# Kernel tuning notes

Measured on AMD Instinct MI355X. Metric: run time of the kernel, lower is better.

The kernel has to match this reference:

```python
import jax, jax.numpy as jnp
import numpy as np

B, S, D, H, FF = 2, 2048, 512, 8, 2048
DK = D // H
EPS = 1e-5


def layer_norm(x, g, b):
    mu = jnp.mean(x, axis=-1, keepdims=True)
    var = jnp.mean((x - mu) ** 2, axis=-1, keepdims=True)
    return (x - mu) / jnp.sqrt(var + EPS) * g + b


def split_heads(x):  # [B,S,D] -> [B,H,S,DK]
    b, s, _ = x.shape
    return x.reshape(b, s, H, DK).transpose(0, 2, 1, 3)


def merge_heads(x):  # [B,H,S,DK] -> [B,S,D]
    b, h, s, dk = x.shape
    return x.transpose(0, 2, 1, 3).reshape(b, s, h * dk)


def mha(q_in, kv, in_w, in_b, out_w, out_b):
    # torch nn.MultiheadAttention, batch_first, eval mode (no dropout)
    Wq, Wk, Wv = in_w[:D], in_w[D:2 * D], in_w[2 * D:]
    bq, bk, bv = in_b[:D], in_b[D:2 * D], in_b[2 * D:]
    q = split_heads(q_in @ Wq.T + bq)
    k = split_heads(kv @ Wk.T + bk)
    v = split_heads(kv @ Wv.T + bv)
    scores = jnp.einsum('bhqd,bhkd->bhqk', q, k) / jnp.sqrt(jnp.float32(DK))
    attn = jax.nn.softmax(scores, axis=-1)
    out = merge_heads(jnp.einsum('bhqk,bhkd->bhqd', attn, v))
    return out @ out_w.T + out_b


def setup_inputs() -> dict:
    key = jax.random.key(0)
    ks = jax.random.split(key, 32)
    p = lambda k, shape: (jax.random.normal(k, shape, jnp.float32) * 0.02)
    inp = {
        'x_q': jax.random.normal(ks[0], (B, S, D), jnp.float32),
        'x1': jax.random.normal(ks[1], (B, S, D), jnp.float32),
        'x2': jax.random.normal(ks[2], (B, S, D), jnp.float32),
        # causal self-attention projections (no output proj in original)
        'sa_wq': p(ks[3], (D, D)), 'sa_bq': jnp.zeros((D,), jnp.float32),
        'sa_wk': p(ks[4], (D, D)), 'sa_bk': jnp.zeros((D,), jnp.float32),
        'sa_wv': p(ks[5], (D, D)), 'sa_bv': jnp.zeros((D,), jnp.float32),
        'ln1_g': jnp.ones((D,), jnp.float32), 'ln1_b': jnp.zeros((D,), jnp.float32),
        # shared cross-attention (cross_attn used twice in forward)
        'mha_in_w': p(ks[6], (3 * D, D)), 'mha_in_b': jnp.zeros((3 * D,), jnp.float32),
        'mha_out_w': p(ks[7], (D, D)), 'mha_out_b': jnp.zeros((D,), jnp.float32),
        # shared add_norm2 (used twice)
        'ln2_g': jnp.ones((D,), jnp.float32), 'ln2_b': jnp.zeros((D,), jnp.float32),
        # FFN
        'ffn_w1': p(ks[8], (FF, D)), 'ffn_b1': jnp.zeros((FF,), jnp.float32),
        'ffn_w2': p(ks[9], (D, FF)), 'ffn_b2': jnp.zeros((D,), jnp.float32),
        # add_norm3 (final)
        'ln3_g': jnp.ones((D,), jnp.float32), 'ln3_b': jnp.zeros((D,), jnp.float32),
    }
    return inp


def reference(x_q, x1, x2, sa_wq, sa_bq, sa_wk, sa_bk, sa_wv, sa_bv,
              ln1_g, ln1_b, mha_in_w, mha_in_b, mha_out_w, mha_out_b,
              ln2_g, ln2_b, ffn_w1, ffn_b1, ffn_w2, ffn_b2, ln3_g, ln3_b):
    # --- causal self-attention (hand-rolled, masked_fill with -1e9) ---
    q = split_heads(x_q @ sa_wq.T + sa_bq)
    k = split_heads(x_q @ sa_wk.T + sa_bk)
    v = split_heads(x_q @ sa_wv.T + sa_bv)
    scores = jnp.einsum('bhqd,bhkd->bhqk', q, k) / jnp.sqrt(jnp.float32(DK))
    causal = jnp.tril(jnp.ones((S, S), dtype=bool))
    scores = jnp.where(causal[None, None], scores, jnp.float32(-1e9))
    attn = jax.nn.softmax(scores, axis=-1)
    y_sa = merge_heads(jnp.einsum('bhqk,bhkd->bhqd', attn, v))
    y = layer_norm(x_q + y_sa, ln1_g, ln1_b)
    # --- cross-attention 1 (shared weights) + shared add_norm2 ---
    yattn = mha(y, x1, mha_in_w, mha_in_b, mha_out_w, mha_out_b)
    yattn = layer_norm(y + yattn, ln2_g, ln2_b)
    # --- cross-attention 2 (SAME module/weights as cross-attn 1) ---
    yattn2 = mha(yattn, x2, mha_in_w, mha_in_b, mha_out_w, mha_out_b)
    yattn2 = layer_norm(yattn + yattn2, ln2_g, ln2_b)
    # --- FFN + add_norm3 ---
    h = jax.nn.relu(yattn2 @ ffn_w1.T + ffn_b1)
    ff = h @ ffn_w2.T + ffn_b2
    return layer_norm(yattn2 + ff, ln3_g, ln3_b)
```

## Files before the change

kernel.cpp:

```cpp
#include <hip/hip_runtime.h>
#include <hip/hip_bf16.h>

#define S_LEN 2048
#define DMODEL 512
#define NHEAD 8
#define DKH 64
#define FFDIM 2048
#define BATCH 2
#define NROWS (BATCH * S_LEN)

using bf16 = __hip_bfloat16;
typedef __bf16 bf16x8 __attribute__((ext_vector_type(8)));
typedef float floatx4 __attribute__((ext_vector_type(4)));
typedef float floatx16 __attribute__((ext_vector_type(16)));

__device__ inline unsigned short f2bf_bits(float f) {
    union { float f; unsigned u; } c; c.f = f;
    return (unsigned short)((c.u + 0x7FFFu + ((c.u >> 16) & 1u)) >> 16);
}
__device__ inline unsigned pack2bf(float a, float b) {
    return (unsigned)f2bf_bits(a) | ((unsigned)f2bf_bits(b) << 16);
}
__device__ inline unsigned pk2(float a, float b) {
    float2 f; f.x = a; f.y = b;
    __hip_bfloat162 h = __float22bfloat162_rn(f);
    return *(unsigned*)&h;
}

__device__ __forceinline__ void gload_lds16(const bf16* g, bf16* l) {
    __builtin_amdgcn_global_load_lds(
        (const __attribute__((address_space(1))) void*)(const void*)g,
        (__attribute__((address_space(3))) void*)(void*)l, 16, 0, 0);
}

struct CvtSeg { const float* s; bf16* d; int n4; };
struct CvtDesc { CvtSeg seg[12]; };

__launch_bounds__(256)
__global__ void cvt_f32_bf16(CvtDesc desc) {
    const CvtSeg sg = desc.seg[blockIdx.y];
    const int stride = gridDim.x * 256;
    for (int i = blockIdx.x * 256 + threadIdx.x; i < sg.n4; i += stride) {
        const float4 v = ((const float4*)sg.s)[i];
        uint2 o;
        o.x = pack2bf(v.x, v.y);
        o.y = pack2bf(v.z, v.w);
        ((uint2*)sg.d)[i] = o;
    }
}

struct Epi {
    bf16*  outB[3];
    float* outF[3];
    const float* bias[3];
    float scale[3];
    const bf16* A2;
    int a2slab;
    int shift;
    int relu;
};

template <int BM, int BN>
__launch_bounds__(256)
__global__ void gemm2(const bf16* __restrict__ A, const bf16* __restrict__ W,
                      Epi epi, int K)
{
    constexpr int WR = BM / 32;
    constexpr int WC = BN / 32;
    constexpr int SA = BM / 16;
    constexpr int SB = BN / 16;
    constexpr int NG = 2 * (SA + SB);

    __shared__ alignas(16) bf16 As[2][BM][32];
    __shared__ alignas(16) bf16 Bs[2][BN][32];

    const int t = threadIdx.x;
    const int w = t >> 6;
    const int lane = t & 63;
    const int r16 = lane & 15;
    const int quad = lane >> 4;
    const int wm = w >> 1, wn = w & 1;
    const int m0 = blockIdx.x * BM;
    const int n0 = blockIdx.y * BN;

    const bf16* Ause = (epi.A2 && ((n0 >> epi.shift) >= epi.a2slab)) ? epi.A2 : A;

    floatx4 acc[WR][WC];
#pragma unroll
    for (int i = 0; i < WR; i++)
#pragma unroll
        for (int j = 0; j < WC; j++)
#pragma unroll
            for (int e = 0; e < 4; e++) acc[i][j][e] = 0.0f;

    const int grow = lane >> 2;
    const int gcol = (lane & 3) * 8;

    for (int k0 = 0; k0 < K; k0 += 64) {
        __syncthreads();
#pragma unroll
        for (int s = 0; s < NG; s += 4) {
            int sg = s + w;
            int p = 0;
            if (sg >= SA + SB) { p = 1; sg -= SA + SB; }
            const bf16* src;
            bf16* dst;
            if (sg < SA) {
                src = Ause + (size_t)(m0 + sg * 16 + grow) * K + k0 + 32 * p + gcol;
                dst = &As[p][sg * 16][0] + lane * 8;
            } else {
                const int sb = sg - SA;
                src = W + (size_t)(n0 + sb * 16 + grow) * K + k0 + 32 * p + gcol;
                dst = &Bs[p][sb * 16][0] + lane * 8;
            }
            gload_lds16(src, dst);
        }
        __syncthreads();

        bf16x8 af[2][WR], bfr[2][WC];
#pragma unroll
        for (int p = 0; p < 2; p++) {
#pragma unroll
            for (int i = 0; i < WR; i++)
                af[p][i] = *(const bf16x8*)&As[p][wm * (BM / 2) + 16 * i + r16][quad * 8];
#pragma unroll
            for (int j = 0; j < WC; j++)
                bfr[p][j] = *(const bf16x8*)&Bs[p][wn * (BN / 2) + 16 * j + r16][quad * 8];
        }
#pragma unroll
        for (int p = 0; p < 2; p++)
#pragma unroll
            for (int i = 0; i < WR; i++)
#pragma unroll
                for (int j = 0; j < WC; j++)
                    acc[i][j] = __builtin_amdgcn_mfma_f32_16x16x32_bf16(af[p][i], bfr[p][j], acc[i][j], 0, 0, 0);
    }

    const int mask = (1 << epi.shift) - 1;
#pragma unroll
    for (int j = 0; j < WC; j++) {
        const int colb = n0 + wn * (BN / 2) + 16 * j;
        const int sel = __builtin_amdgcn_readfirstlane(colb >> epi.shift);
        const int lcol = (colb & mask) + r16;
        const int ldw = mask + 1;
        const float bv = epi.bias[sel] ? epi.bias[sel][lcol] : 0.0f;
        const float sc = epi.scale[sel];
        bf16* ob = epi.outB[sel];
        float* of = epi.outF[sel];
#pragma unroll
        for (int i = 0; i < WR; i++) {
            const int rowb = m0 + wm * (BM / 2) + 16 * i + 4 * quad;
#pragma unroll
            for (int e = 0; e < 4; e++) {
                float v = (acc[i][j][e] + bv) * sc;
                if (epi.relu) v = fmaxf(v, 0.0f);
                const size_t idx = (size_t)(rowb + e) * ldw + lcol;
                if (of) of[idx] = v;
                if (ob) ob[idx] = __float2bfloat16(v);
            }
        }
    }
}

#define PST 72

__launch_bounds__(256)
__global__ void attn_mfma(const bf16* __restrict__ Qh, const bf16* __restrict__ Kh,
                          const bf16* __restrict__ Vh,
                          float* __restrict__ outF, bf16* __restrict__ outB,
                          int causal)
{
    __shared__ alignas(16) char smem[36864];
    typedef bf16 (*VtT)[64][PST];
    typedef bf16 (*PsT)[32][PST];
    VtT Vt = (VtT)smem;
    PsT Ps = (PsT)(smem + 18432);
    typedef float (*MshT)[64][34];
    MshT Msh = (MshT)smem;

    const int t = threadIdx.x;
    const int w = t >> 6;
    const int lane = t & 63;
    const int c32 = lane & 31;
    const int hi = lane >> 5;
    const int pair = t >> 7;
    const int qg = w & 1;
    const int pl = t & 127;
    const int bh = blockIdx.y;
    const int b = bh >> 3, h = bh & 7;
    const int q0 = blockIdx.x * 64;
    const size_t rowbase = (size_t)b * S_LEN;
    const int hoff = h * DKH;

    bf16x8 qf[4];
    {
        const bf16* qp = Qh + (rowbase + q0 + 32 * qg + c32) * DMODEL + hoff + 8 * hi;
#pragma unroll
        for (int tt = 0; tt < 4; tt++) qf[tt] = *(const bf16x8*)(qp + 16 * tt);
    }

    floatx16 o0, o1;
#pragma unroll
    for (int e = 0; e < 16; e++) { o0[e] = 0.0f; o1[e] = 0.0f; }
    float m = -3e38f, l = 0.0f;

    const int rq = pl & 15;
    const int c8 = ((pl >> 4) & 7) * 8;

    const int nchunk = causal ? (q0 / 64 + 1) : (S_LEN / 64);
    const int nIter = (nchunk + 1) >> 1;

    bf16x8 kf0[4], kf1[4];
    if (pair < nchunk) {
        const bf16* kp = Kh + (rowbase + pair * 64 + c32) * DMODEL + hoff + 8 * hi;
#pragma unroll
        for (int tt = 0; tt < 4; tt++) {
            kf0[tt] = *(const bf16x8*)(kp + 16 * tt);
            kf1[tt] = *(const bf16x8*)(kp + (size_t)32 * DMODEL + 16 * tt);
        }
    }

    for (int it = 0; it < nIter; it++) {
        const int ch = 2 * it + pair;
        const bool active = ch < nchunk;
        const int kb = ch * 64;
        __syncthreads();
        if (active) {
            union { uint4 u; unsigned short s[8]; } r0, r1, r2, r3;
            const bf16* vb = Vh + (rowbase + kb + 4 * rq) * DMODEL + hoff + c8;
            r0.u = *(const uint4*)(vb);
            r1.u = *(const uint4*)(vb + DMODEL);
            r2.u = *(const uint4*)(vb + 2 * DMODEL);
            r3.u = *(const uint4*)(vb + 3 * DMODEL);
#pragma unroll
            for (int j = 0; j < 8; j++) {
                ushort4 pk = { r0.s[j], r1.s[j], r2.s[j], r3.s[j] };
                *(ushort4*)&Vt[pair][c8 + j][4 * rq] = pk;
            }
        }

        if (active) {
            floatx16 s0, s1;
#pragma unroll
            for (int e = 0; e < 16; e++) { s0[e] = 0.0f; s1[e] = 0.0f; }
#pragma unroll
            for (int tt = 0; tt < 4; tt++) {
                s0 = __builtin_amdgcn_mfma_f32_32x32x16_bf16(kf0[tt], qf[tt], s0, 0, 0, 0);
                s1 = __builtin_amdgcn_mfma_f32_32x32x16_bf16(kf1[tt], qf[tt], s1, 0, 0, 0);
            }

            const int chn = ch + 2;
            if (chn < nchunk) {
                const bf16* kp = Kh + (rowbase + chn * 64 + c32) * DMODEL + hoff + 8 * hi;
#pragma unroll
                for (int tt = 0; tt < 4; tt++) {
                    kf0[tt] = *(const bf16x8*)(kp + 16 * tt);
                    kf1[tt] = *(const bf16x8*)(kp + (size_t)32 * DMODEL + 16 * tt);
                }
            }

            if (causal && kb == q0) {
                const int qq = 32 * qg + c32;
#pragma unroll
                for (int r = 0; r < 16; r++) {
                    const int kl = (r & 3) + 8 * (r >> 2) + 4 * hi;
                    if (kl > qq) s0[r] = -3e38f;
                    if (kl + 32 > qq) s1[r] = -3e38f;
                }
            }

            float mc = -3e38f;
#pragma unroll
            for (int r = 0; r < 16; r++) mc = fmaxf(mc, fmaxf(s0[r], s1[r]));
            mc = fmaxf(mc, __shfl_xor(mc, 32, 64));
            const float mold = m;
            const float mn = fmaxf(m, mc);
            const float alpha = __expf(mold - mn);
            m = mn;

            float lc = 0.0f;
#pragma unroll
            for (int g = 0; g < 4; g++) {
                float p0 = __expf(s0[4 * g + 0] - mn), p1 = __expf(s0[4 * g + 1] - mn);
                float p2 = __expf(s0[4 * g + 2] - mn), p3 = __expf(s0[4 * g + 3] - mn);
                lc += (p0 + p1) + (p2 + p3);
                uint2 pw; pw.x = pk2(p0, p1); pw.y = pk2(p2, p3);
                *(uint2*)&Ps[w][c32][8 * g + 4 * hi] = pw;
                p0 = __expf(s1[4 * g + 0] - mn); p1 = __expf(s1[4 * g + 1] - mn);
                p2 = __expf(s1[4 * g + 2] - mn); p3 = __expf(s1[4 * g + 3] - mn);
                lc += (p0 + p1) + (p2 + p3);
                uint2 pw1; pw1.x = pk2(p0, p1); pw1.y = pk2(p2, p3);
                *(uint2*)&Ps[w][c32][32 + 8 * g + 4 * hi] = pw1;
            }
            lc += __shfl_xor(lc, 32, 64);
            l = l * alpha + lc;

            if (!__all(mn == mold)) {
#pragma unroll
                for (int r = 0; r < 16; r++) {
                    const float a = __shfl(alpha, (r & 3) + 8 * (r >> 2) + 4 * hi, 64);
                    o0[r] *= a; o1[r] *= a;
                }
            }
        }

        __syncthreads();

        if (active) {
#pragma unroll
            for (int tt = 0; tt < 4; tt++) {
                const bf16x8 pf = *(const bf16x8*)&Ps[w][c32][16 * tt + 8 * hi];
                const bf16x8 v0 = *(const bf16x8*)&Vt[pair][c32][16 * tt + 8 * hi];
                const bf16x8 v1 = *(const bf16x8*)&Vt[pair][32 + c32][16 * tt + 8 * hi];
                o0 = __builtin_amdgcn_mfma_f32_32x32x16_bf16(pf, v0, o0, 0, 0, 0);
                o1 = __builtin_amdgcn_mfma_f32_32x32x16_bf16(pf, v1, o1, 0, 0, 0);
            }
        }
    }

    __syncthreads();
    if (pair == 1) {
        float* dst = &Msh[qg][lane][0];
        dst[0] = m; dst[1] = l;
#pragma unroll
        for (int r = 0; r < 16; r++) { dst[2 + r] = o0[r]; dst[18 + r] = o1[r]; }
    }
    __syncthreads();
    if (pair == 0) {
        const float* src = &Msh[qg][lane][0];
        const float m_b = src[0], l_b = src[1];
        const float mt = fmaxf(m, m_b);
        const float sA = __expf(m - mt);
        const float sB = __expf(m_b - mt);
        const float lt = l * sA + l_b * sB;
#pragma unroll
        for (int r = 0; r < 16; r++) {
            const int ql = (r & 3) + 8 * (r >> 2) + 4 * hi;
            const float sAr = __shfl(sA, ql, 64);
            const float sBr = __shfl(sB, ql, 64);
            const float li = 1.0f / __shfl(lt, ql, 64);
            const float v0 = (o0[r] * sAr + src[2 + r] * sBr) * li;
            const float v1 = (o1[r] * sAr + src[18 + r] * sBr) * li;
            const size_t idx = (rowbase + q0 + 32 * qg + ql) * DMODEL + hoff + c32;
            if (outF) { outF[idx] = v0; outF[idx + 32] = v1; }
            if (outB) { outB[idx] = __float2bfloat16(v0); outB[idx + 32] = __float2bfloat16(v1); }
        }
    }
}

__launch_bounds__(256)
__global__ void ln_kernel(const float* __restrict__ xmain,
                          const float* __restrict__ resF, const bf16* __restrict__ resB,
                          const float* __restrict__ g, const float* __restrict__ bb,
                          float* __restrict__ outF, bf16* __restrict__ outB)
{
    const int row = blockIdx.x;
    const int t = threadIdx.x;
    const size_t base = (size_t)row * DMODEL;

    float x0 = xmain[base + t];
    float x1 = xmain[base + t + 256];
    if (resF) { x0 += resF[base + t]; x1 += resF[base + t + 256]; }
    if (resB) { x0 += __bfloat162float(resB[base + t]); x1 += __bfloat162float(resB[base + t + 256]); }

    __shared__ float sred[4];
    float s = x0 + x1;
#pragma unroll
    for (int off = 32; off > 0; off >>= 1) s += __shfl_down(s, off);
    if ((t & 63) == 0) sred[t >> 6] = s;
    __syncthreads();
    const float mu = (sred[0] + sred[1] + sred[2] + sred[3]) * (1.0f / DMODEL);

    const float d0 = x0 - mu, d1 = x1 - mu;
    float sv = d0 * d0 + d1 * d1;
#pragma unroll
    for (int off = 32; off > 0; off >>= 1) sv += __shfl_down(sv, off);
    __syncthreads();
    if ((t & 63) == 0) sred[t >> 6] = sv;
    __syncthreads();
    const float var = (sred[0] + sred[1] + sred[2] + sred[3]) * (1.0f / DMODEL);
    const float rstd = rsqrtf(var + 1e-5f);

    const float y0 = d0 * rstd * g[t] + bb[t];
    const float y1 = d1 * rstd * g[t + 256] + bb[t + 256];
    if (outF) { outF[base + t] = y0; outF[base + t + 256] = y1; }
    if (outB) { outB[base + t] = __float2bfloat16(y0); outB[base + t + 256] = __float2bfloat16(y1); }
}

extern "C" void kernel_launch(void* const* d_in, const int* in_sizes, int n_in,
                              void* d_out, int out_size, void* d_ws, size_t ws_size,
                              hipStream_t stream)
{
    const float* x_q       = (const float*)d_in[0];
    const float* x1        = (const float*)d_in[1];
    const float* x2        = (const float*)d_in[2];
    const float* sa_wq     = (const float*)d_in[3];
    const float* sa_bq     = (const float*)d_in[4];
    const float* sa_wk     = (const float*)d_in[5];
    const float* sa_bk     = (const float*)d_in[6];
    const float* sa_wv     = (const float*)d_in[7];
    const float* sa_bv     = (const float*)d_in[8];
    const float* ln1_g     = (const float*)d_in[9];
    const float* ln1_b     = (const float*)d_in[10];
    const float* mha_in_w  = (const float*)d_in[11];
    const float* mha_in_b  = (const float*)d_in[12];
    const float* mha_out_w = (const float*)d_in[13];
    const float* mha_out_b = (const float*)d_in[14];
    const float* ln2_g     = (const float*)d_in[15];
    const float* ln2_b     = (const float*)d_in[16];
    const float* ffn_w1    = (const float*)d_in[17];
    const float* ffn_b1    = (const float*)d_in[18];
    const float* ffn_w2    = (const float*)d_in[19];
    const float* ffn_b2    = (const float*)d_in[20];
    const float* ln3_g     = (const float*)d_in[21];
    const float* ln3_b     = (const float*)d_in[22];

    char* ws = (char*)d_ws;
    const size_t MB = 1024 * 1024;
    const size_t KB = 1024;
    bf16*  q16  = (bf16*)(ws + 0 * MB);
    bf16*  k16  = (bf16*)(ws + 4 * MB);
    bf16*  v16  = (bf16*)(ws + 8 * MB);
    bf16*  a16  = (bf16*)(ws + 12 * MB);
    float* tmp  = (float*)(ws + 16 * MB);
    bf16*  y16  = (bf16*)(ws + 24 * MB);
    bf16*  ya16 = (bf16*)(ws + 28 * MB);
    bf16*  ya2  = (bf16*)(ws + 32 * MB);
    bf16*  xq16 = (bf16*)(ws + 36 * MB);
    bf16*  x116 = (bf16*)(ws + 40 * MB);
    bf16*  x216 = (bf16*)(ws + 44 * MB);
    bf16*  w_sa_qkv = (bf16*)(ws + 48 * MB);
    bf16*  w_in   = (bf16*)(ws + 49 * MB + 512 * KB);
    bf16*  w_out  = (bf16*)(ws + 51 * MB);
    bf16*  w_f1   = (bf16*)(ws + 51 * MB + 512 * KB);
    bf16*  w_f2   = (bf16*)(ws + 53 * MB + 512 * KB);
    bf16*  h16    = (bf16*)(ws + 0 * MB);

    const int DD = DMODEL * DMODEL;
    CvtDesc cd;
    cd.seg[0]  = { x_q,       xq16,        (NROWS * DMODEL) / 4 };
    cd.seg[1]  = { x1,        x116,        (NROWS * DMODEL) / 4 };
    cd.seg[2]  = { x2,        x216,        (NROWS * DMODEL) / 4 };
    cd.seg[3]  = { sa_wq,     w_sa_qkv,           DD / 4 };
    cd.seg[4]  = { sa_wk,     w_sa_qkv + DD,      DD / 4 };
    cd.seg[5]  = { sa_wv,     w_sa_qkv + 2 * DD,  DD / 4 };
    cd.seg[6]  = { mha_in_w,  w_in,   3 * DD / 4 };
    cd.seg[7]  = { mha_out_w, w_out,  DD / 4 };
    cd.seg[8]  = { ffn_w1,    w_f1,   (FFDIM * DMODEL) / 4 };
    cd.seg[9]  = { ffn_w2,    w_f2,   (FFDIM * DMODEL) / 4 };
    cd.seg[10] = { x_q,       xq16,   0 };
    cd.seg[11] = { x_q,       xq16,   0 };
    cvt_f32_bf16<<<dim3(64, 10), 256, 0, stream>>>(cd);

    const dim3 blk(256);
    const dim3 agrid(S_LEN / 64, BATCH * NHEAD);

    Epi eQKV = {};
    eQKV.outB[0] = q16; eQKV.outB[1] = k16; eQKV.outB[2] = v16;
    eQKV.bias[0] = sa_bq; eQKV.bias[1] = sa_bk; eQKV.bias[2] = sa_bv;
    eQKV.scale[0] = 0.125f; eQKV.scale[1] = 1.0f; eQKV.scale[2] = 1.0f;
    eQKV.shift = 9;

    Epi eX1 = {};
    eX1.outB[0] = q16; eX1.outB[1] = k16; eX1.outB[2] = v16;
    eX1.bias[0] = mha_in_b; eX1.bias[1] = mha_in_b + DMODEL; eX1.bias[2] = mha_in_b + 2 * DMODEL;
    eX1.scale[0] = 0.125f; eX1.scale[1] = 1.0f; eX1.scale[2] = 1.0f;
    eX1.A2 = x116; eX1.a2slab = 1; eX1.shift = 9;

    Epi eX2 = eX1;
    eX2.A2 = x216;

    Epi eOut = {};
    eOut.outF[0] = tmp; eOut.bias[0] = mha_out_b; eOut.scale[0] = 1.0f; eOut.shift = 9;

    Epi eF1 = {};
    eF1.outB[0] = h16; eF1.bias[0] = ffn_b1; eF1.scale[0] = 1.0f;
    eF1.shift = 11; eF1.relu = 1;

    Epi eF2 = {};
    eF2.outF[0] = tmp; eF2.bias[0] = ffn_b2; eF2.scale[0] = 1.0f; eF2.shift = 9;

    gemm2<64, 64><<<dim3(64, 24), blk, 0, stream>>>(xq16, w_sa_qkv, eQKV, DMODEL);
    attn_mfma<<<agrid, blk, 0, stream>>>(q16, k16, v16, tmp, nullptr, 1);
    ln_kernel<<<NROWS, blk, 0, stream>>>(tmp, x_q, nullptr, ln1_g, ln1_b, nullptr, y16);

    gemm2<64, 64><<<dim3(64, 24), blk, 0, stream>>>(y16, w_in, eX1, DMODEL);
    attn_mfma<<<agrid, blk, 0, stream>>>(q16, k16, v16, nullptr, a16, 0);
    gemm2<64, 64><<<dim3(64, 8), blk, 0, stream>>>(a16, w_out, eOut, DMODEL);
    ln_kernel<<<NROWS, blk, 0, stream>>>(tmp, nullptr, y16, ln2_g, ln2_b, nullptr, ya16);

    gemm2<64, 64><<<dim3(64, 24), blk, 0, stream>>>(ya16, w_in, eX2, DMODEL);
    attn_mfma<<<agrid, blk, 0, stream>>>(q16, k16, v16, nullptr, a16, 0);
    gemm2<64, 64><<<dim3(64, 8), blk, 0, stream>>>(a16, w_out, eOut, DMODEL);
    ln_kernel<<<NROWS, blk, 0, stream>>>(tmp, nullptr, ya16, ln2_g, ln2_b, nullptr, ya2);

    gemm2<128, 128><<<dim3(32, 16), blk, 0, stream>>>(ya2, w_f1, eF1, DMODEL);
    gemm2<64, 64><<<dim3(64, 8), blk, 0, stream>>>(h16, w_f2, eF2, FFDIM);
    ln_kernel<<<NROWS, blk, 0, stream>>>(tmp, nullptr, ya2, ln3_g, ln3_b, (float*)d_out, nullptr);
}
```

Before: 441.3 us.

## Split attention KV loop four ways per block and keep P in registers

The attention kernel moves from 256 to 512 threads, so four wave pairs each take every fourth 64-key chunk instead of two pairs alternating. The partial softmax states of all four are then merged through shared memory at the end. The P tile is no longer staged through shared memory: the MFMA A-operand fragment is rebuilt from registers with cross-half lane shuffles. This is meant to add parallelism within each block and cut LDS traffic, at the cost of a larger shared-memory footprint, more register pressure under the 512-thread launch bound, and a heavier final merge.

```diff
diff --git a/kernel.cpp b/kernel.cpp
--- a/kernel.cpp
+++ b/kernel.cpp
@@ -164,27 +164,24 @@
 
 #define PST 72
 
-__launch_bounds__(256)
+__launch_bounds__(512, 4)
 __global__ void attn_mfma(const bf16* __restrict__ Qh, const bf16* __restrict__ Kh,
                           const bf16* __restrict__ Vh,
                           float* __restrict__ outF, bf16* __restrict__ outB,
                           int causal)
 {
-    __shared__ alignas(16) char smem[36864];
+    __shared__ alignas(16) char smem[52224];
     typedef bf16 (*VtT)[64][PST];
-    typedef bf16 (*PsT)[32][PST];
     VtT Vt = (VtT)smem;
-    PsT Ps = (PsT)(smem + 18432);
-    typedef float (*MshT)[64][34];
+    typedef float (*MshT)[3][64][34];
     MshT Msh = (MshT)smem;
 
     const int t = threadIdx.x;
-    const int w = t >> 6;
     const int lane = t & 63;
     const int c32 = lane & 31;
     const int hi = lane >> 5;
-    const int pair = t >> 7;
-    const int qg = w & 1;
+    const int sp = t >> 7;
+    const int qg = (t >> 6) & 1;
     const int pl = t & 127;
     const int bh = blockIdx.y;
     const int b = bh >> 3, h = bh & 7;
@@ -208,11 +205,11 @@
     const int c8 = ((pl >> 4) & 7) * 8;
 
     const int nchunk = causal ? (q0 / 64 + 1) : (S_LEN / 64);
-    const int nIter = (nchunk + 1) >> 1;
+    const int nIter = (nchunk + 3) >> 2;
 
     bf16x8 kf0[4], kf1[4];
-    if (pair < nchunk) {
-        const bf16* kp = Kh + (rowbase + pair * 64 + c32) * DMODEL + hoff + 8 * hi;
+    if (sp < nchunk) {
+        const bf16* kp = Kh + (rowbase + sp * 64 + c32) * DMODEL + hoff + 8 * hi;
 #pragma unroll
         for (int tt = 0; tt < 4; tt++) {
             kf0[tt] = *(const bf16x8*)(kp + 16 * tt);
@@ -221,7 +218,7 @@
     }
 
     for (int it = 0; it < nIter; it++) {
-        const int ch = 2 * it + pair;
+        const int ch = 4 * it + sp;
         const bool active = ch < nchunk;
         const int kb = ch * 64;
         __syncthreads();
@@ -235,9 +232,11 @@
 #pragma unroll
             for (int j = 0; j < 8; j++) {
                 ushort4 pk = { r0.s[j], r1.s[j], r2.s[j], r3.s[j] };
-                *(ushort4*)&Vt[pair][c8 + j][4 * rq] = pk;
-            }
-        }
+                *(ushort4*)&Vt[sp][c8 + j][4 * rq] = pk;
+            }
+        }
+
+        uint2 pgrp[2][4];
 
         if (active) {
             floatx16 s0, s1;
@@ -249,7 +248,7 @@
                 s1 = __builtin_amdgcn_mfma_f32_32x32x16_bf16(kf1[tt], qf[tt], s1, 0, 0, 0);
             }
 
-            const int chn = ch + 2;
+            const int chn = ch + 4;
             if (chn < nchunk) {
                 const bf16* kp = Kh + (rowbase + chn * 64 + c32) * DMODEL + hoff + 8 * hi;
 #pragma unroll
@@ -284,13 +283,11 @@
                 float p0 = __expf(s0[4 * g + 0] - mn), p1 = __expf(s0[4 * g + 1] - mn);
                 float p2 = __expf(s0[4 * g + 2] - mn), p3 = __expf(s0[4 * g + 3] - mn);
                 lc += (p0 + p1) + (p2 + p3);
-                uint2 pw; pw.x = pk2(p0, p1); pw.y = pk2(p2, p3);
-                *(uint2*)&Ps[w][c32][8 * g + 4 * hi] = pw;
+                pgrp[0][g].x = pk2(p0, p1); pgrp[0][g].y = pk2(p2, p3);
                 p0 = __expf(s1[4 * g + 0] - mn); p1 = __expf(s1[4 * g + 1] - mn);
                 p2 = __expf(s1[4 * g + 2] - mn); p3 = __expf(s1[4 * g + 3] - mn);
                 lc += (p0 + p1) + (p2 + p3);
-                uint2 pw1; pw1.x = pk2(p0, p1); pw1.y = pk2(p2, p3);
-                *(uint2*)&Ps[w][c32][32 + 8 * g + 4 * hi] = pw1;
+                pgrp[1][g].x = pk2(p0, p1); pgrp[1][g].y = pk2(p2, p3);
             }
             lc += __shfl_xor(lc, 32, 64);
             l = l * alpha + lc;
@@ -309,38 +306,57 @@
         if (active) {
 #pragma unroll
             for (int tt = 0; tt < 4; tt++) {
-                const bf16x8 pf = *(const bf16x8*)&Ps[w][c32][16 * tt + 8 * hi];
-                const bf16x8 v0 = *(const bf16x8*)&Vt[pair][c32][16 * tt + 8 * hi];
-                const bf16x8 v1 = *(const bf16x8*)&Vt[pair][32 + c32][16 * tt + 8 * hi];
-                o0 = __builtin_amdgcn_mfma_f32_32x32x16_bf16(pf, v0, o0, 0, 0, 0);
-                o1 = __builtin_amdgcn_mfma_f32_32x32x16_bf16(pf, v1, o1, 0, 0, 0);
+                const int sel = tt >> 1;
+                const int t2 = tt & 1;
+                const uint2 ge = pgrp[sel][2 * t2];
+                const uint2 go = pgrp[sel][2 * t2 + 1];
+                uint2 swe, swo;
+                swe.x = __shfl_xor((int)ge.x, 32, 64); swe.y = __shfl_xor((int)ge.y, 32, 64);
+                swo.x = __shfl_xor((int)go.x, 32, 64); swo.y = __shfl_xor((int)go.y, 32, 64);
+                union { unsigned u[4]; bf16x8 v; } fr;
+                fr.u[0] = hi ? swo.x : ge.x;
+                fr.u[1] = hi ? swo.y : ge.y;
+                fr.u[2] = hi ? go.x : swe.x;
+                fr.u[3] = hi ? go.y : swe.y;
+                const bf16x8 v0 = *(const bf16x8*)&Vt[sp][c32][16 * tt + 8 * hi];
+                const bf16x8 v1 = *(const bf16x8*)&Vt[sp][32 + c32][16 * tt + 8 * hi];
+                o0 = __builtin_amdgcn_mfma_f32_32x32x16_bf16(fr.v, v0, o0, 0, 0, 0);
+                o1 = __builtin_amdgcn_mfma_f32_32x32x16_bf16(fr.v, v1, o1, 0, 0, 0);
             }
         }
     }
 
     __syncthreads();
-    if (pair == 1) {
-        float* dst = &Msh[qg][lane][0];
+    if (sp > 0) {
+        float* dst = &Msh[qg][sp - 1][lane][0];
         dst[0] = m; dst[1] = l;
 #pragma unroll
         for (int r = 0; r < 16; r++) { dst[2 + r] = o0[r]; dst[18 + r] = o1[r]; }
     }
     __syncthreads();
-    if (pair == 0) {
-        const float* src = &Msh[qg][lane][0];
-        const float m_b = src[0], l_b = src[1];
-        const float mt = fmaxf(m, m_b);
+    if (sp == 0) {
+        const float* p1 = &Msh[qg][0][lane][0];
+        const float* p2 = &Msh[qg][1][lane][0];
+        const float* p3 = &Msh[qg][2][lane][0];
+        const float m1 = p1[0], l1 = p1[1];
+        const float m2 = p2[0], l2 = p2[1];
+        const float m3 = p3[0], l3 = p3[1];
+        const float mt = fmaxf(fmaxf(m, m1), fmaxf(m2, m3));
         const float sA = __expf(m - mt);
-        const float sB = __expf(m_b - mt);
-        const float lt = l * sA + l_b * sB;
+        const float s1c = __expf(m1 - mt);
+        const float s2c = __expf(m2 - mt);
+        const float s3c = __expf(m3 - mt);
+        const float lt = l * sA + l1 * s1c + l2 * s2c + l3 * s3c;
 #pragma unroll
         for (int r = 0; r < 16; r++) {
             const int ql = (r & 3) + 8 * (r >> 2) + 4 * hi;
-            const float sAr = __shfl(sA, ql, 64);
-            const float sBr = __shfl(sB, ql, 64);
+            const float aA = __shfl(sA, ql, 64);
+            const float a1 = __shfl(s1c, ql, 64);
+            const float a2 = __shfl(s2c, ql, 64);
+            const float a3 = __shfl(s3c, ql, 64);
             const float li = 1.0f / __shfl(lt, ql, 64);
-            const float v0 = (o0[r] * sAr + src[2 + r] * sBr) * li;
-            const float v1 = (o1[r] * sAr + src[18 + r] * sBr) * li;
+            const float v0 = (o0[r] * aA + p1[2 + r] * a1 + p2[2 + r] * a2 + p3[2 + r] * a3) * li;
+            const float v1 = (o1[r] * aA + p1[18 + r] * a1 + p2[18 + r] * a2 + p3[18 + r] * a3) * li;
             const size_t idx = (rowbase + q0 + 32 * qg + ql) * DMODEL + hoff + c32;
             if (outF) { outF[idx] = v0; outF[idx + 32] = v1; }
             if (outB) { outB[idx] = __float2bfloat16(v0); outB[idx + 32] = __float2bfloat16(v1); }
@@ -453,6 +469,7 @@
     cvt_f32_bf16<<<dim3(64, 10), 256, 0, stream>>>(cd);
 
     const dim3 blk(256);
+    const dim3 ablk(512);
     const dim3 agrid(S_LEN / 64, BATCH * NHEAD);
 
     Epi eQKV = {};
@@ -481,16 +498,16 @@
     eF2.outF[0] = tmp; eF2.bias[0] = ffn_b2; eF2.scale[0] = 1.0f; eF2.shift = 9;
 
     gemm2<64, 64><<<dim3(64, 24), blk, 0, stream>>>(xq16, w_sa_qkv, eQKV, DMODEL);
-    attn_mfma<<<agrid, blk, 0, stream>>>(q16, k16, v16, tmp, nullptr, 1);
+    attn_mfma<<<agrid, ablk, 0, stream>>>(q16, k16, v16, tmp, nullptr, 1);
     ln_kernel<<<NROWS, blk, 0, stream>>>(tmp, x_q, nullptr, ln1_g, ln1_b, nullptr, y16);
 
     gemm2<64, 64><<<dim3(64, 24), blk, 0, stream>>>(y16, w_in, eX1, DMODEL);
-    attn_mfma<<<agrid, blk, 0, stream>>>(q16, k16, v16, nullptr, a16, 0);
+    attn_mfma<<<agrid, ablk, 0, stream>>>(q16, k16, v16, nullptr, a16, 0);
     gemm2<64, 64><<<dim3(64, 8), blk, 0, stream>>>(a16, w_out, eOut, DMODEL);
     ln_kernel<<<NROWS, blk, 0, stream>>>(tmp, nullptr, y16, ln2_g, ln2_b, nullptr, ya16);
 
     gemm2<64, 64><<<dim3(64, 24), blk, 0, stream>>>(ya16, w_in, eX2, DMODEL);
-    attn_mfma<<<agrid, blk, 0, stream>>>(q16, k16, v16, nullptr, a16, 0);
+    attn_mfma<<<agrid, ablk, 0, stream>>>(q16, k16, v16, nullptr, a16, 0);
     gemm2<64, 64><<<dim3(64, 8), blk, 0, stream>>>(a16, w_out, eOut, DMODEL);
     ln_kernel<<<NROWS, blk, 0, stream>>>(tmp, nullptr, ya16, ln2_g, ln2_b, nullptr, ya2);
 
```

Measured after the change: 667.1 us. 1.51x slower.
